# Kernel optimization log

Hardware: AMD Instinct MI355X
Metric: run time of the kernel (lower is better)

The kernel has to match this reference:

```python
import jax, jax.numpy as jnp
import numpy as np

N_NODES = 40000
N_EDGES = 640000
D_FEAT = 128


def setup_inputs() -> dict:
    key = jax.random.key(0)
    k1, k2, k3, k4 = jax.random.split(key, 4)
    rows = jax.random.randint(k1, (N_EDGES,), 0, N_NODES, dtype=jnp.int32)
    cols = jax.random.randint(k2, (N_EDGES,), 0, N_NODES, dtype=jnp.int32)
    vals = jax.random.uniform(k3, (N_EDGES,), dtype=jnp.float32)
    annotations = jax.random.normal(k4, (N_NODES, D_FEAT), dtype=jnp.float32)
    return {"rows": rows, "cols": cols, "vals": vals, "annotations": annotations}


def reference(rows, cols, vals, annotations):
    # out = adjacent @ annotations, with adjacent given in COO form:
    # adjacent[rows[e], cols[e]] = vals[e].
    # SpMM as gather -> scale -> segment_sum over destination rows.
    gathered = annotations[cols] * vals[:, None]          # [E, d]
    out = jax.ops.segment_sum(gathered, rows, num_segments=N_NODES)  # [N, d]
    return out
```

## Files before the change

### kernel.cpp

```cpp
#include <hip/hip_runtime.h>


constexpr int N_NODES = 40000;
constexpr int N_EDGES = 640000;
constexpr int D_FEAT  = 128;
constexpr int CAP     = 32;
constexpr int OVF_CAP = 16384;
constexpr int CSTR    = 16;

constexpr int SCAT_BLOCKS = N_EDGES / 256;
constexpr int CONV_BLOCKS = (N_NODES * D_FEAT / 8) / 256;

constexpr size_t WS_CURSOR = 0;
constexpr size_t WS_OVFCNT = 2560000;
constexpr size_t WS_OVF    = 2560256;
constexpr size_t WS_ANNB   = 2822400;
constexpr size_t WS_PAIRS  = 13062400;
constexpr size_t WS_ZERO   = 2560256;
constexpr size_t WS_NEEDED = 23302400;

typedef int      v2i __attribute__((ext_vector_type(2)));
typedef float    v2f __attribute__((ext_vector_type(2)));
typedef float    v4f __attribute__((ext_vector_type(4)));
typedef unsigned v4u __attribute__((ext_vector_type(4)));

__device__ __forceinline__ unsigned f2b_rne(float f) {
    unsigned b = __float_as_uint(f);
    return (b + 0x7fffu + ((b >> 16) & 1u)) >> 16;
}

__global__ __launch_bounds__(256) void build_kernel(
    const int*   __restrict__ rows,
    const int*   __restrict__ cols,
    const float* __restrict__ vals,
    const float* __restrict__ ann,
    unsigned*    __restrict__ annb,
    int* __restrict__ cursor, v2i* __restrict__ pairs,
    int* __restrict__ ovfcnt, int4* __restrict__ ovf)
{
    if (blockIdx.x < SCAT_BLOCKS) {
        int e = blockIdx.x * 256 + threadIdx.x;
        int   r = __builtin_nontemporal_load(rows + e);
        int   c = __builtin_nontemporal_load(cols + e);
        float v = __builtin_nontemporal_load(vals + e);
        int slot = atomicAdd(&cursor[r * CSTR], 1);
        if (slot < CAP) {
            v2i p;
            p.x = c;
            p.y = __float_as_int(v);
            pairs[r * CAP + slot] = p;
        } else {
            int o = atomicAdd(ovfcnt, 1);
            if (o < OVF_CAP) ovf[o] = make_int4(r, c, __float_as_int(v), 0);
        }
    } else {
        int t = (blockIdx.x - SCAT_BLOCKS) * 256 + threadIdx.x;
        v4f f0 = __builtin_nontemporal_load(reinterpret_cast<const v4f*>(ann) + 2 * t);
        v4f f1 = __builtin_nontemporal_load(reinterpret_cast<const v4f*>(ann) + 2 * t + 1);
        v4u o;
        o.x = f2b_rne(f0.x) | (f2b_rne(f0.y) << 16);
        o.y = f2b_rne(f0.z) | (f2b_rne(f0.w) << 16);
        o.z = f2b_rne(f1.x) | (f2b_rne(f1.y) << 16);
        o.w = f2b_rne(f1.z) | (f2b_rne(f1.w) << 16);
        reinterpret_cast<v4u*>(annb)[t] = o;
    }
}

__global__ __launch_bounds__(256) void pull_kernel(
    const unsigned* __restrict__ annb,
    const int*      __restrict__ cursor,
    const v2i*      __restrict__ pairs,
    const int*      __restrict__ ovfcnt,
    const int4*     __restrict__ ovf,
    float*          __restrict__ out)
{
    int r    = (blockIdx.x * blockDim.x + threadIdx.x) >> 6;
    int lane = threadIdx.x & 63;

    int cntr = cursor[r * CSTR];
    int cnt  = cntr > CAP ? CAP : cntr;

    int2 pr = make_int2(0, 0);
    if (lane < cnt) {
        v2i p = __builtin_nontemporal_load(pairs + (r * CAP + lane));
        pr.x = p.x;
        pr.y = p.y;
    }

    float2 acc = make_float2(0.f, 0.f);
    int nb = (cnt + 7) & ~7;
    for (int j = 0; j < nb; j += 8) {
        #pragma unroll
        for (int k = 0; k < 8; k++) {
            int      c = __shfl(pr.x, j + k, 64);
            float    v = __int_as_float(__shfl(pr.y, j + k, 64));
            unsigned p = annb[c * (D_FEAT / 2) + lane];
            acc.x += v * __uint_as_float(p << 16);
            acc.y += v * __uint_as_float(p & 0xffff0000u);
        }
    }

    if (cntr > CAP) {
        int n = *ovfcnt;
        n = n > OVF_CAP ? OVF_CAP : n;
        for (int i = 0; i < n; i++) {
            int4 e = ovf[i];
            if (e.x == r) {
                unsigned p = annb[e.y * (D_FEAT / 2) + lane];
                float    v = __int_as_float(e.z);
                acc.x += v * __uint_as_float(p << 16);
                acc.y += v * __uint_as_float(p & 0xffff0000u);
            }
        }
    }

    v2f o;
    o.x = acc.x;
    o.y = acc.y;
    __builtin_nontemporal_store(
        o, reinterpret_cast<v2f*>(out) + ((size_t)r * (D_FEAT / 2) + lane));
}

__global__ __launch_bounds__(256) void spmm_scatter_kernel(
    const int*   __restrict__ rows,
    const int*   __restrict__ cols,
    const float* __restrict__ vals,
    const float* __restrict__ ann,
    float*       __restrict__ out)
{
    int t = blockIdx.x * blockDim.x + threadIdx.x;
    int e = t >> 5;
    if (e >= N_EDGES) return;
    int lane = t & 31;
    int   r = rows[e];
    int   c = cols[e];
    float v = vals[e];
    float4 a = reinterpret_cast<const float4*>(ann)[(size_t)c * (D_FEAT / 4) + lane];
    float* o = out + (size_t)r * D_FEAT + lane * 4;
    unsafeAtomicAdd(o + 0, v * a.x);
    unsafeAtomicAdd(o + 1, v * a.y);
    unsafeAtomicAdd(o + 2, v * a.z);
    unsafeAtomicAdd(o + 3, v * a.w);
}

extern "C" void kernel_launch(void* const* d_in, const int* in_sizes, int n_in,
                              void* d_out, int out_size, void* d_ws, size_t ws_size,
                              hipStream_t stream) {
    const int*   rows = (const int*)  d_in[0];
    const int*   cols = (const int*)  d_in[1];
    const float* vals = (const float*)d_in[2];
    const float* ann  = (const float*)d_in[3];
    float*       out  = (float*)      d_out;

    if (ws_size < WS_NEEDED) {
        hipMemsetAsync(out, 0, (size_t)out_size * sizeof(float), stream);
        const long long total_threads = (long long)N_EDGES * 32;
        spmm_scatter_kernel<<<dim3((unsigned)((total_threads + 255) / 256)),
                              dim3(256), 0, stream>>>(rows, cols, vals, ann, out);
        return;
    }

    char*     ws     = (char*)d_ws;
    int*      cursor = (int*)     (ws + WS_CURSOR);
    int*      ovfcnt = (int*)     (ws + WS_OVFCNT);
    int4*     ovf    = (int4*)    (ws + WS_OVF);
    unsigned* annb   = (unsigned*)(ws + WS_ANNB);
    v2i*      pairs  = (v2i*)     (ws + WS_PAIRS);

    hipMemsetAsync(cursor, 0, WS_ZERO, stream);

    build_kernel<<<dim3(SCAT_BLOCKS + CONV_BLOCKS), dim3(256), 0, stream>>>(
        rows, cols, vals, ann, annb, cursor, pairs, ovfcnt, ovf);

    const long long pull_threads = (long long)N_NODES * 64;
    pull_kernel<<<dim3((unsigned)((pull_threads + 255) / 256)), dim3(256), 0, stream>>>(
        annb, cursor, pairs, ovfcnt, ovf, out);
}
```

Before: 139.0 us.

## Partition edge scatter and pull rows by XCD to keep atomics and pairs local

Measured after the change: 135.7 us (median of 2 runs). 2.4% less time.

```diff
diff --git a/kernel.cpp b/kernel.cpp
--- a/kernel.cpp
+++ b/kernel.cpp
@@ -8,7 +8,12 @@
 constexpr int OVF_CAP = 16384;
 constexpr int CSTR    = 16;
 
-constexpr int SCAT_BLOCKS = N_EDGES / 256;
+constexpr int NXCD      = 8;
+constexpr int PART_ROWS = N_NODES / NXCD;
+constexpr int EPT       = 10;
+constexpr int CHUNK     = 256 * EPT;
+constexpr int NCHUNK    = N_EDGES / CHUNK;
+constexpr int SCAT_BLOCKS = NCHUNK * NXCD;
 constexpr int CONV_BLOCKS = (N_NODES * D_FEAT / 8) / 256;
 
 constexpr size_t WS_CURSOR = 0;
@@ -39,19 +44,33 @@
     int* __restrict__ ovfcnt, int4* __restrict__ ovf)
 {
     if (blockIdx.x < SCAT_BLOCKS) {
-        int e = blockIdx.x * 256 + threadIdx.x;
-        int   r = __builtin_nontemporal_load(rows + e);
-        int   c = __builtin_nontemporal_load(cols + e);
-        float v = __builtin_nontemporal_load(vals + e);
-        int slot = atomicAdd(&cursor[r * CSTR], 1);
-        if (slot < CAP) {
-            v2i p;
-            p.x = c;
-            p.y = __float_as_int(v);
-            pairs[r * CAP + slot] = p;
-        } else {
-            int o = atomicAdd(ovfcnt, 1);
-            if (o < OVF_CAP) ovf[o] = make_int4(r, c, __float_as_int(v), 0);
+        int p     = blockIdx.x & 7;
+        int chunk = blockIdx.x >> 3;
+        int e0    = chunk * CHUNK + threadIdx.x;
+
+        int   r[EPT], c[EPT];
+        float v[EPT];
+        #pragma unroll
+        for (int i = 0; i < EPT; i++) {
+            int e = e0 + i * 256;
+            r[i] = __builtin_nontemporal_load(rows + e);
+            c[i] = __builtin_nontemporal_load(cols + e);
+            v[i] = __builtin_nontemporal_load(vals + e);
+        }
+        #pragma unroll
+        for (int i = 0; i < EPT; i++) {
+            if (r[i] / PART_ROWS != p) continue;
+            int slot = atomicAdd(&cursor[r[i] * CSTR], 1);
+            if (slot < CAP) {
+                v2i q;
+                q.x = c[i];
+                q.y = __float_as_int(v[i]);
+                pairs[r[i] * CAP + slot] = q;
+            } else {
+                int o = atomicAdd(ovfcnt, 1);
+                if (o < OVF_CAP)
+                    ovf[o] = make_int4(r[i], c[i], __float_as_int(v[i]), 0);
+            }
         }
     } else {
         int t = (blockIdx.x - SCAT_BLOCKS) * 256 + threadIdx.x;
@@ -74,7 +93,9 @@
     const int4*     __restrict__ ovf,
     float*          __restrict__ out)
 {
-    int r    = (blockIdx.x * blockDim.x + threadIdx.x) >> 6;
+    int B = blockIdx.x;
+    int L = (B & 7) * 1250 + (B >> 3);
+    int r    = L * 4 + (threadIdx.x >> 6);
     int lane = threadIdx.x & 63;
 
     int cntr = cursor[r * CSTR];
@@ -82,7 +103,7 @@
 
     int2 pr = make_int2(0, 0);
     if (lane < cnt) {
-        v2i p = __builtin_nontemporal_load(pairs + (r * CAP + lane));
+        v2i p = pairs[r * CAP + lane];
         pr.x = p.x;
         pr.y = p.y;
     }
```
